# Optimization experiments

Hardware: AMD Instinct MI355X
Metric: run time of the kernel (lower is better)

The kernel has to match this reference:

```python
import jax, jax.numpy as jnp
import numpy as np

ALPHA, BETA, GAMMA, EPS = 10.0, 0.1, 1.0, 1e-20
MARK_INDEX = jnp.array([0, 29, 88, 117])

B, S, D, P, C, V = 64, 128, 2048, 118, 2, 512


def setup_inputs() -> dict:
    key = jax.random.key(0)
    ks = jax.random.split(key, 9)
    qy_raw = jax.random.uniform(ks[4], (B, S, V), dtype=jnp.float32)
    qy = qy_raw / jnp.sum(qy_raw, axis=-1, keepdims=True)  # probabilities
    return {
        "zs": jax.random.normal(ks[0], (B, S, D), dtype=jnp.float32),
        "rzs": jax.random.normal(ks[1], (B, S, D), dtype=jnp.float32),
        "pts": jax.random.normal(ks[2], (B, S, P, C), dtype=jnp.float32),
        "pts_gt": jax.random.normal(ks[3], (B, S, P, C), dtype=jnp.float32),
        "qy": qy,
        "logits": jax.random.normal(ks[5], (B, S, V), dtype=jnp.float32),
        "best": jax.random.normal(ks[6], (B, P, C), dtype=jnp.float32),
        "best_gt": jax.random.normal(ks[7], (B, P, C), dtype=jnp.float32),
        "mapping": jax.random.randint(ks[8], (B, S), 0, S, dtype=jnp.int64),
        "vector_dims": V,
    }


def _mse(a, b):
    return jnp.mean(jnp.square(a - b))


def reference(zs, rzs, pts, pts_gt, qy, logits, best, best_gt, mapping, vector_dims):
    # KL divergence vs uniform categorical over vector_dims
    log_g = jnp.log(jnp.float32(1.0) / vector_dims)
    kld = jnp.mean(jnp.sum(qy * (jnp.log(qy + EPS) - log_g), axis=-1))

    best_pts_loss = _mse(best, best_gt) + ALPHA * _mse(
        best[..., MARK_INDEX, :], best_gt[..., MARK_INDEX, :]
    )

    # mapping-indexed gather along dim 1 (vectorized form of the double loop;
    # per-element mse means are all over equal-sized slices, so the summed/
    # averaged loop equals a single global mean over the gathered tensors)
    rz_m = jnp.take_along_axis(rzs, mapping[:, :, None], axis=1)          # [B,S,D]
    x_m = jnp.take_along_axis(pts, mapping[:, :, None, None], axis=1)    # [B,S,P,C]
    recon = _mse(rz_m, zs)
    disk = _mse(x_m, pts_gt)
    landmark = _mse(x_m[..., MARK_INDEX, :], pts_gt[..., MARK_INDEX, :])
    pts_loss = disk + ALPHA * landmark

    total = BETA * kld + GAMMA * recon + pts_loss + best_pts_loss
    return total
```

## Files before the change

kernel.cpp:

```cpp
#include <hip/hip_runtime.h>
#include <math.h>

#define NB 64
#define NS 128
#define ND 2048
#define NP 118
#define NC 2
#define NV 512

constexpr int RECON_BLOCKS = 2048;
constexpr int KLD_BLOCKS   = 512;
constexpr int PTS_BLOCKS   = 512;
constexpr int BEST_BLOCKS  = 16;
constexpr int TOTAL_BLOCKS = RECON_BLOCKS + KLD_BLOCKS + PTS_BLOCKS + BEST_BLOCKS;

#define LOAD_FENCE() asm volatile("" ::: "memory")

__global__ __launch_bounds__(256) void cq_main(
    const float* __restrict__ zs, const float* __restrict__ rzs,
    const float* __restrict__ pts, const float* __restrict__ pts_gt,
    const float* __restrict__ qy,
    const float* __restrict__ best, const float* __restrict__ best_gt,
    const int* __restrict__ mapping, const int* __restrict__ vd,
    float* __restrict__ partials)
{
    const float w_recon = 1.0f / 16777216.0f;
    const float w_kld   = 0.1f / 8192.0f;
    const float w_disk  = 1.0f / 1933312.0f;
    const float w_land  = 10.0f / 65536.0f;
    const float w_best  = 1.0f / 15104.0f;
    const float w_bland = 10.0f / 512.0f;

    const int t   = threadIdx.x;
    const int blk = blockIdx.x;
    float acc = 0.0f;

    __shared__ int mrow[16];

    if (blk < RECON_BLOCKS) {
        const int r0 = blk << 2;
        const int b  = r0 >> 7;
        const int m0 = mapping[r0];
        const int m1 = mapping[r0 + 1];
        const int m2 = mapping[r0 + 2];
        const int m3 = mapping[r0 + 3];
        const float4* zb4 = (const float4*)zs  + ((size_t)r0 << 9);
        const float4* rz4 = (const float4*)rzs + ((size_t)b << 16);
        const int rb0 = m0 << 9, rb1 = m1 << 9, rb2 = m2 << 9, rb3 = m3 << 9;

        float4 z[8], r[8];
        #pragma unroll
        for (int k = 0; k < 8; ++k) z[k] = zb4[t + (k << 8)];
        r[0] = rz4[rb0 + t];       r[1] = rz4[rb0 + 256 + t];
        r[2] = rz4[rb1 + t];       r[3] = rz4[rb1 + 256 + t];
        r[4] = rz4[rb2 + t];       r[5] = rz4[rb2 + 256 + t];
        r[6] = rz4[rb3 + t];       r[7] = rz4[rb3 + 256 + t];
        LOAD_FENCE();

        float s = 0.0f;
        #pragma unroll
        for (int k = 0; k < 8; ++k) {
            float dx = r[k].x - z[k].x, dy = r[k].y - z[k].y;
            float dz = r[k].z - z[k].z, dw = r[k].w - z[k].w;
            s += dx*dx + dy*dy + dz*dz + dw*dw;
        }
        acc = w_recon * s;
    } else if (blk < RECON_BLOCKS + KLD_BLOCKS) {
        const int rb = blk - RECON_BLOCKS;
        const float log_g = -__logf((float)vd[0]);
        const float4* qp = (const float4*)qy + ((size_t)rb << 11) + t;
        float4 q[8];
        #pragma unroll
        for (int k = 0; k < 8; ++k) q[k] = qp[k * 256];
        LOAD_FENCE();
        float s = 0.0f;
        #pragma unroll
        for (int k = 0; k < 8; ++k) {
            s += q[k].x * (__logf(q[k].x + 1e-20f) - log_g)
               + q[k].y * (__logf(q[k].y + 1e-20f) - log_g)
               + q[k].z * (__logf(q[k].z + 1e-20f) - log_g)
               + q[k].w * (__logf(q[k].w + 1e-20f) - log_g);
        }
        acc = w_kld * s;
    } else if (blk < RECON_BLOCKS + KLD_BLOCKS + PTS_BLOCKS) {
        const int rb = blk - (RECON_BLOCKS + KLD_BLOCKS);
        if (t < 16) mrow[t] = mapping[(rb << 4) + t];
        __syncthreads();
        const int bs_base = rb << 4;
        float4 x[4], g[4];
        int pbase[4];
        #pragma unroll
        for (int j = 0; j < 4; ++j) {
            const int w = t + j * 256;
            const unsigned rl = (unsigned)w / 59u;
            const int qo = w - (int)rl * 59;
            const bool valid = (w < 944);
            const int rl_c = valid ? (int)rl : 0;
            const int bs = bs_base + rl_c;
            const int b  = bs >> 7;
            const int m  = mrow[rl_c];
            const size_t xi = (size_t)((b << 7) + m) * 236 + (qo << 2);
            const size_t gi = (size_t)(rb * 944 + w) << 2;
            pbase[j] = valid ? (qo << 1) : -100;
            x[j] = valid ? *(const float4*)(pts    + xi) : make_float4(0,0,0,0);
            g[j] = valid ? *(const float4*)(pts_gt + gi) : make_float4(0,0,0,0);
        }
        LOAD_FENCE();
        #pragma unroll
        for (int j = 0; j < 4; ++j) {
            const float* xp = (const float*)&x[j];
            const float* gp = (const float*)&g[j];
            #pragma unroll
            for (int jj = 0; jj < 4; ++jj) {
                const int p = pbase[j] + (jj >> 1);
                const bool marked = (p == 0) | (p == 29) | (p == 88) | (p == 117);
                const float wgt = w_disk + (marked ? w_land : 0.0f);
                const float d = xp[jj] - gp[jj];
                acc += wgt * d * d;
            }
        }
    } else {
        const int db = blk - (RECON_BLOCKS + KLD_BLOCKS + PTS_BLOCKS);
        if (t < 236) {
            const int l = db * 236 + t;
            const unsigned bq = (unsigned)l / 59u;
            const int qo = l - (int)bq * 59;
            const float4 x = *(const float4*)(best    + ((size_t)l << 2));
            const float4 g = *(const float4*)(best_gt + ((size_t)l << 2));
            const float* xp = (const float*)&x;
            const float* gp = (const float*)&g;
            const int p2 = qo << 1;
            #pragma unroll
            for (int jj = 0; jj < 4; ++jj) {
                const int p = p2 + (jj >> 1);
                const bool marked = (p == 0) | (p == 29) | (p == 88) | (p == 117);
                const float wgt = w_best + (marked ? w_bland : 0.0f);
                const float d = xp[jj] - gp[jj];
                acc += wgt * d * d;
            }
        }
    }

    #pragma unroll
    for (int o = 32; o > 0; o >>= 1) acc += __shfl_down(acc, o, 64);

    __shared__ float wsum[4];
    const int lane = t & 63;
    const int wave = t >> 6;
    if (lane == 0) wsum[wave] = acc;
    __syncthreads();
    if (t == 0) partials[blk] = wsum[0] + wsum[1] + wsum[2] + wsum[3];
}

__global__ __launch_bounds__(256) void cq_reduce(
    const float* __restrict__ partials, float* __restrict__ out)
{
    const int t = threadIdx.x;
    float acc = 0.0f;
    for (int i = t; i < TOTAL_BLOCKS; i += 256) acc += partials[i];
    #pragma unroll
    for (int o = 32; o > 0; o >>= 1) acc += __shfl_down(acc, o, 64);
    __shared__ float wsum[4];
    if ((t & 63) == 0) wsum[t >> 6] = acc;
    __syncthreads();
    if (t == 0) out[0] = wsum[0] + wsum[1] + wsum[2] + wsum[3];
}

extern "C" void kernel_launch(void* const* d_in, const int* in_sizes, int n_in,
                              void* d_out, int out_size, void* d_ws, size_t ws_size,
                              hipStream_t stream) {
    const float* zs      = (const float*)d_in[0];
    const float* rzs     = (const float*)d_in[1];
    const float* pts     = (const float*)d_in[2];
    const float* pts_gt  = (const float*)d_in[3];
    const float* qy      = (const float*)d_in[4];
    const float* best    = (const float*)d_in[6];
    const float* best_gt = (const float*)d_in[7];
    const int*   mapping = (const int*)d_in[8];
    const int*   vd      = (const int*)d_in[9];
    float* out      = (float*)d_out;
    float* partials = (float*)d_ws;

    cq_main<<<TOTAL_BLOCKS, 256, 0, stream>>>(zs, rzs, pts, pts_gt, qy,
                                              best, best_gt, mapping, vd, partials);
    cq_reduce<<<1, 256, 0, stream>>>(partials, out);
}
```

Measured before the change: 189.6 us.

## Make recon and KLD waves persistent with double-buffered software-pipelined loads

```diff
diff --git a/kernel.cpp b/kernel.cpp
--- a/kernel.cpp
+++ b/kernel.cpp
@@ -8,13 +8,49 @@
 #define NC 2
 #define NV 512
 
-constexpr int RECON_BLOCKS = 2048;
-constexpr int KLD_BLOCKS   = 512;
+constexpr int RECON_BLOCKS = 512;
+constexpr int KLD_BLOCKS   = 128;
 constexpr int PTS_BLOCKS   = 512;
 constexpr int BEST_BLOCKS  = 16;
 constexpr int TOTAL_BLOCKS = RECON_BLOCKS + KLD_BLOCKS + PTS_BLOCKS + BEST_BLOCKS;
 
-#define LOAD_FENCE() asm volatile("" ::: "memory")
+constexpr int RECON_WAVES = RECON_BLOCKS * 4;
+constexpr int RECON_UNITS = (NB*NS*ND/4) / 256;
+constexpr int KLD_WAVES   = KLD_BLOCKS * 4;
+constexpr int KLD_UNITS   = (NB*NS*NV/4) / 256;
+
+
+#define RISSUE(Z, R, uu, mm) do {                                          \
+    const float4* zp_ = z4 + (((size_t)(uu)) << 8) + lane;                 \
+    Z[0] = zp_[0]; Z[1] = zp_[64]; Z[2] = zp_[128]; Z[3] = zp_[192];       \
+    const float4* rp_ = r4 + (size_t)((((uu) >> 8) << 16) + ((mm) << 9)    \
+                                      + (((uu) & 1) << 8)) + lane;         \
+    R[0] = rp_[0]; R[1] = rp_[64]; R[2] = rp_[128]; R[3] = rp_[192];       \
+  } while (0)
+
+#define RCONS(Z, R, sacc) do {                                             \
+    _Pragma("unroll")                                                      \
+    for (int j_ = 0; j_ < 4; ++j_) {                                       \
+        float dx = R[j_].x - Z[j_].x, dy = R[j_].y - Z[j_].y;              \
+        float dz = R[j_].z - Z[j_].z, dw = R[j_].w - Z[j_].w;              \
+        sacc += dx*dx + dy*dy + dz*dz + dw*dw;                             \
+    }                                                                      \
+  } while (0)
+
+#define QISSUE(Q, uu) do {                                                 \
+    const float4* qp_ = q4 + (((size_t)(uu)) << 8) + lane;                 \
+    Q[0] = qp_[0]; Q[1] = qp_[64]; Q[2] = qp_[128]; Q[3] = qp_[192];       \
+  } while (0)
+
+#define QCONS(Q, sacc) do {                                                \
+    _Pragma("unroll")                                                      \
+    for (int j_ = 0; j_ < 4; ++j_) {                                       \
+        sacc += Q[j_].x * (__logf(Q[j_].x + 1e-20f) - log_g)               \
+              + Q[j_].y * (__logf(Q[j_].y + 1e-20f) - log_g)               \
+              + Q[j_].z * (__logf(Q[j_].z + 1e-20f) - log_g)               \
+              + Q[j_].w * (__logf(Q[j_].w + 1e-20f) - log_g);              \
+    }                                                                      \
+  } while (0)
 
 __global__ __launch_bounds__(256) void cq_main(
     const float* __restrict__ zs, const float* __restrict__ rzs,
@@ -31,55 +67,67 @@
     const float w_best  = 1.0f / 15104.0f;
     const float w_bland = 10.0f / 512.0f;
 
-    const int t   = threadIdx.x;
-    const int blk = blockIdx.x;
+    const int t    = threadIdx.x;
+    const int blk  = blockIdx.x;
+    const int lane = t & 63;
     float acc = 0.0f;
 
     __shared__ int mrow[16];
 
     if (blk < RECON_BLOCKS) {
-        const int r0 = blk << 2;
-        const int b  = r0 >> 7;
-        const int m0 = mapping[r0];
-        const int m1 = mapping[r0 + 1];
-        const int m2 = mapping[r0 + 2];
-        const int m3 = mapping[r0 + 3];
-        const float4* zb4 = (const float4*)zs  + ((size_t)r0 << 9);
-        const float4* rz4 = (const float4*)rzs + ((size_t)b << 16);
-        const int rb0 = m0 << 9, rb1 = m1 << 9, rb2 = m2 << 9, rb3 = m3 << 9;
-
-        float4 z[8], r[8];
-        #pragma unroll
-        for (int k = 0; k < 8; ++k) z[k] = zb4[t + (k << 8)];
-        r[0] = rz4[rb0 + t];       r[1] = rz4[rb0 + 256 + t];
-        r[2] = rz4[rb1 + t];       r[3] = rz4[rb1 + 256 + t];
-        r[4] = rz4[rb2 + t];       r[5] = rz4[rb2 + 256 + t];
-        r[6] = rz4[rb3 + t];       r[7] = rz4[rb3 + 256 + t];
-        LOAD_FENCE();
-
+        const int gw = (blk << 2) + (t >> 6);
+        const float4* z4 = (const float4*)zs;
+        const float4* r4 = (const float4*)rzs;
+        float4 zA[4], rA[4], zB[4], rB[4];
         float s = 0.0f;
-        #pragma unroll
-        for (int k = 0; k < 8; ++k) {
-            float dx = r[k].x - z[k].x, dy = r[k].y - z[k].y;
-            float dz = r[k].z - z[k].z, dw = r[k].w - z[k].w;
-            s += dx*dx + dy*dy + dz*dz + dw*dw;
+
+        int u = gw;
+        int mA = mapping[u >> 1];
+        RISSUE(zA, rA, u, mA);
+        int mn = mapping[(u + RECON_WAVES) >> 1];
+        #pragma unroll 1
+        for (int i = 0; i < 3; ++i) {
+            const int ub = u + RECON_WAVES;
+            RISSUE(zB, rB, ub, mn);
+            const int mn2 = mapping[(ub + RECON_WAVES) >> 1];
+            RCONS(zA, rA, s);
+            const int ua = ub + RECON_WAVES;
+            RISSUE(zA, rA, ua, mn2);
+            mn = mapping[(ua + RECON_WAVES) >> 1];
+            RCONS(zB, rB, s);
+            u = ua;
+        }
+        {
+            const int ub = u + RECON_WAVES;
+            RISSUE(zB, rB, ub, mn);
+            RCONS(zA, rA, s);
+            RCONS(zB, rB, s);
         }
         acc = w_recon * s;
     } else if (blk < RECON_BLOCKS + KLD_BLOCKS) {
-        const int rb = blk - RECON_BLOCKS;
+        const int gw = ((blk - RECON_BLOCKS) << 2) + (t >> 6);
         const float log_g = -__logf((float)vd[0]);
-        const float4* qp = (const float4*)qy + ((size_t)rb << 11) + t;
-        float4 q[8];
-        #pragma unroll
-        for (int k = 0; k < 8; ++k) q[k] = qp[k * 256];
-        LOAD_FENCE();
+        const float4* q4 = (const float4*)qy;
+        float4 qA[4], qB[4];
         float s = 0.0f;
-        #pragma unroll
-        for (int k = 0; k < 8; ++k) {
-            s += q[k].x * (__logf(q[k].x + 1e-20f) - log_g)
-               + q[k].y * (__logf(q[k].y + 1e-20f) - log_g)
-               + q[k].z * (__logf(q[k].z + 1e-20f) - log_g)
-               + q[k].w * (__logf(q[k].w + 1e-20f) - log_g);
+
+        int u = gw;
+        QISSUE(qA, u);
+        #pragma unroll 1
+        for (int i = 0; i < 3; ++i) {
+            const int ub = u + KLD_WAVES;
+            QISSUE(qB, ub);
+            QCONS(qA, s);
+            const int ua = ub + KLD_WAVES;
+            QISSUE(qA, ua);
+            QCONS(qB, s);
+            u = ua;
+        }
+        {
+            const int ub = u + KLD_WAVES;
+            QISSUE(qB, ub);
+            QCONS(qA, s);
+            QCONS(qB, s);
         }
         acc = w_kld * s;
     } else if (blk < RECON_BLOCKS + KLD_BLOCKS + PTS_BLOCKS) {
@@ -105,7 +153,6 @@
             x[j] = valid ? *(const float4*)(pts    + xi) : make_float4(0,0,0,0);
             g[j] = valid ? *(const float4*)(pts_gt + gi) : make_float4(0,0,0,0);
         }
-        LOAD_FENCE();
         #pragma unroll
         for (int j = 0; j < 4; ++j) {
             const float* xp = (const float*)&x[j];
@@ -145,9 +192,8 @@
     for (int o = 32; o > 0; o >>= 1) acc += __shfl_down(acc, o, 64);
 
     __shared__ float wsum[4];
-    const int lane = t & 63;
     const int wave = t >> 6;
-    if (lane == 0) wsum[wave] = acc;
+    if ((t & 63) == 0) wsum[wave] = acc;
     __syncthreads();
     if (t == 0) partials[blk] = wsum[0] + wsum[1] + wsum[2] + wsum[3];
 }
```

Measured after the change: 191.5 us. Within noise of the previous version (+1.0%).
